# Kernel optimization log

Measured on AMD Instinct MI355X. Metric: run time of the kernel, lower is better.

The kernel has to match this reference:

```python
import jax, jax.numpy as jnp
import numpy as np

B, L, D = 4, 2048, 1024
H = 4096          # hidden_units = 4*D
E = 8             # n_expert
K = 2             # n_expert_activated


def setup_inputs() -> dict:
    key = jax.random.key(0)
    k_x, k_g, k_w1, k_w2 = jax.random.split(key, 4)
    xs = jax.random.normal(k_x, (B, L, D), dtype=jnp.float32)
    gate_w = jax.random.normal(k_g, (E, D), dtype=jnp.float32) * 0.02   # Linear(D->E), no bias
    w1 = jax.random.normal(k_w1, (E, D, H), dtype=jnp.float32) * 0.02   # per-expert w_1 (bias=False)
    w2 = jax.random.normal(k_w2, (E, H, D), dtype=jnp.float32) * 0.02   # per-expert w_2 (bias=False)
    return {"xs": xs, "gate_w": gate_w, "w1": w1, "w2": w2}


def reference(xs, gate_w, w1, w2):
    b, l, d = xs.shape
    x = xs.reshape(-1, d)                                  # (N, D)
    n = x.shape[0]
    router = jnp.einsum('nd,ed->ne', x, gate_w)            # (N, E)
    logits, sel = jax.lax.top_k(router, K)                 # (N, K) each
    weights = jax.nn.softmax(logits.astype(jnp.float32), axis=-1).astype(x.dtype)
    # dense (N, E) combine weights: zero for unselected experts
    dense_w = jnp.zeros((n, E), dtype=x.dtype).at[jnp.arange(n)[:, None], sel].set(weights)
    # dense dispatch: run every expert on every token, zero-weight unselected.
    # Same math as the per-expert gather/scatter loop (dropout inactive at eval).
    h = jax.nn.relu(jnp.einsum('nd,edh->neh', x, w1))      # (N, E, H)
    out = jnp.einsum('neh,ehd,ne->nd', h, w2, dense_w)     # (N, D)
    return out.reshape(b, l, d)
```

## Files before the change

kernel.cpp:

```cpp
#include <hip/hip_runtime.h>
#include <hip/hip_bf16.h>

#define NTOK   8192
#define DDIM   1024
#define HDIM   4096
#define NEXP   8
#define CAP    8192
#define NSLOT  (NTOK * 2)

#define BM 128
#define BN 128
#define BK 64
#define KPAD 72

typedef __attribute__((ext_vector_type(8))) short bf16x8;
typedef __attribute__((ext_vector_type(4))) float f32x4;

__global__ __launch_bounds__(64) void router_kernel(
    const float* __restrict__ xs, const float* __restrict__ gw,
    int* __restrict__ counts, int* __restrict__ toklist, float* __restrict__ wglist)
{
    const int n = blockIdx.x;
    const int lane = threadIdx.x;
    const float* xrow = xs + (size_t)n * DDIM;
    float xv[16];
#pragma unroll
    for (int j = 0; j < 16; ++j) xv[j] = xrow[lane + 64 * j];
    float logit[NEXP];
#pragma unroll
    for (int e = 0; e < NEXP; ++e) {
        float p = 0.f;
        const float* gr = gw + e * DDIM;
#pragma unroll
        for (int j = 0; j < 16; ++j) p += xv[j] * gr[lane + 64 * j];
#pragma unroll
        for (int off = 32; off >= 1; off >>= 1) p += __shfl_xor(p, off);
        logit[e] = p;
    }
    if (lane == 0) {
        int i0 = 0;
#pragma unroll
        for (int e = 1; e < NEXP; ++e) if (logit[e] > logit[i0]) i0 = e;
        int i1 = (i0 == 0) ? 1 : 0;
#pragma unroll
        for (int e = 0; e < NEXP; ++e) if (e != i0 && logit[e] > logit[i1]) i1 = e;
        float ex = expf(logit[i1] - logit[i0]);
        float w0 = 1.f / (1.f + ex);
        float w1 = ex * w0;
        int p0 = atomicAdd(&counts[i0], 1);
        toklist[i0 * CAP + p0] = n;
        wglist[i0 * CAP + p0] = w0;
        int p1 = atomicAdd(&counts[i1], 1);
        toklist[i1 * CAP + p1] = n;
        wglist[i1 * CAP + p1] = w1;
    }
}

__global__ void prefix_kernel(const int* __restrict__ counts, int* __restrict__ base)
{
    if (threadIdx.x == 0 && blockIdx.x == 0) {
        int s = 0;
        for (int e = 0; e < NEXP; ++e) { base[e] = s; s += counts[e]; }
    }
}

__global__ __launch_bounds__(256) void cvt_xs_kernel(
    const float* __restrict__ xs, __hip_bfloat16* __restrict__ xsb)
{
    const size_t i = ((size_t)blockIdx.x * 256 + threadIdx.x) * 8;
    const float4 a = *(const float4*)(xs + i);
    const float4 b = *(const float4*)(xs + i + 4);
    __hip_bfloat16 o[8];
    o[0] = __float2bfloat16(a.x); o[1] = __float2bfloat16(a.y);
    o[2] = __float2bfloat16(a.z); o[3] = __float2bfloat16(a.w);
    o[4] = __float2bfloat16(b.x); o[5] = __float2bfloat16(b.y);
    o[6] = __float2bfloat16(b.z); o[7] = __float2bfloat16(b.w);
    *(bf16x8*)(xsb + i) = *(bf16x8*)o;
}

__global__ __launch_bounds__(256) void transpose_bf16_kernel(
    const float* __restrict__ src, __hip_bfloat16* __restrict__ dst, int R, int C)
{
    __shared__ __hip_bfloat16 t[64][65];
    const int e = blockIdx.z;
    src += (size_t)e * R * C;
    dst += (size_t)e * R * C;
    const int r0 = blockIdx.y * 64, c0 = blockIdx.x * 64;
    const int tid = threadIdx.x;
#pragma unroll
    for (int i = 0; i < 16; ++i) {
        int lin = tid + 256 * i;
        int r = lin >> 6, c = lin & 63;
        t[r][c] = __float2bfloat16(src[(size_t)(r0 + r) * C + c0 + c]);
    }
    __syncthreads();
#pragma unroll
    for (int i = 0; i < 16; ++i) {
        int lin = tid + 256 * i;
        int c = lin >> 6, r = lin & 63;
        dst[(size_t)(c0 + c) * R + r0 + r] = t[r][c];
    }
}

__global__ __launch_bounds__(256) void gemm1_kernel(
    const __hip_bfloat16* __restrict__ xsb, const __hip_bfloat16* __restrict__ w1t,
    const int* __restrict__ counts, const int* __restrict__ base,
    const int* __restrict__ toklist, __hip_bfloat16* __restrict__ h)
{
    const int e = blockIdx.z;
    const int cnt = counts[e];
    const int m0 = blockIdx.y * BM;
    if (m0 >= cnt) return;
    const int n0 = blockIdx.x * BN;

    __shared__ __align__(16) __hip_bfloat16 As[BM * KPAD];
    __shared__ __align__(16) __hip_bfloat16 Bs[BN * KPAD];
    __shared__ int tok_s[BM];

    const int tid = threadIdx.x;
    if (tid < BM) {
        int m = m0 + tid;
        tok_s[tid] = (m < cnt) ? toklist[e * CAP + m] : -1;
    }
    __syncthreads();

    f32x4 acc[4][4];
#pragma unroll
    for (int i = 0; i < 4; ++i)
#pragma unroll
        for (int j = 0; j < 4; ++j) acc[i][j] = (f32x4){0.f, 0.f, 0.f, 0.f};

    const int wave = tid >> 6;
    const int lane = tid & 63;
    const int wm = (wave >> 1) * 64;
    const int wn = (wave & 1) * 64;
    const int l15 = lane & 15;
    const int quad = lane >> 4;
    const int srow = tid >> 3;
    const int soct = (tid & 7) * 8;
    const __hip_bfloat16* w1e = w1t + (size_t)e * HDIM * DDIM;

    for (int k0 = 0; k0 < DDIM; k0 += BK) {
#pragma unroll
        for (int rr = 0; rr < 4; ++rr) {
            int m = srow + rr * 32;
            int t = tok_s[m];
            bf16x8 v = {0, 0, 0, 0, 0, 0, 0, 0};
            if (t >= 0) v = *(const bf16x8*)(xsb + (size_t)t * DDIM + k0 + soct);
            *(bf16x8*)(As + m * KPAD + soct) = v;
        }
#pragma unroll
        for (int rr = 0; rr < 4; ++rr) {
            int n = srow + rr * 32;
            bf16x8 v = *(const bf16x8*)(w1e + (size_t)(n0 + n) * DDIM + k0 + soct);
            *(bf16x8*)(Bs + n * KPAD + soct) = v;
        }
        __syncthreads();
#pragma unroll
        for (int kk = 0; kk < 2; ++kk) {
            bf16x8 a[4], b[4];
#pragma unroll
            for (int i = 0; i < 4; ++i)
                a[i] = *(const bf16x8*)(As + (wm + i * 16 + l15) * KPAD + kk * 32 + quad * 8);
#pragma unroll
            for (int j = 0; j < 4; ++j)
                b[j] = *(const bf16x8*)(Bs + (wn + j * 16 + l15) * KPAD + kk * 32 + quad * 8);
#pragma unroll
            for (int i = 0; i < 4; ++i)
#pragma unroll
                for (int j = 0; j < 4; ++j)
                    acc[i][j] = __builtin_amdgcn_mfma_f32_16x16x32_bf16(a[i], b[j], acc[i][j], 0, 0, 0);
        }
        __syncthreads();
    }

    const int slot0 = base[e] + m0;
#pragma unroll
    for (int i = 0; i < 4; ++i) {
#pragma unroll
        for (int r = 0; r < 4; ++r) {
            int row = wm + i * 16 + quad * 4 + r;
            if (m0 + row < cnt) {
                size_t hrow = (size_t)(slot0 + row) * HDIM + n0 + wn;
#pragma unroll
                for (int j = 0; j < 4; ++j)
                    h[hrow + j * 16 + l15] = __float2bfloat16(fmaxf(acc[i][j][r], 0.f));
            }
        }
    }
}

__global__ __launch_bounds__(256) void gemm2_kernel(
    const __hip_bfloat16* __restrict__ h, const __hip_bfloat16* __restrict__ w2t,
    const int* __restrict__ counts, const int* __restrict__ base,
    const int* __restrict__ toklist, const float* __restrict__ wglist,
    float* __restrict__ out)
{
    const int e = blockIdx.z;
    const int cnt = counts[e];
    const int m0 = blockIdx.y * BM;
    if (m0 >= cnt) return;
    const int n0 = blockIdx.x * BN;

    __shared__ __align__(16) __hip_bfloat16 As[BM * KPAD];
    __shared__ __align__(16) __hip_bfloat16 Bs[BN * KPAD];
    __shared__ int   tok_s[BM];
    __shared__ float wg_s[BM];

    const int tid = threadIdx.x;
    if (tid < BM) {
        int m = m0 + tid;
        tok_s[tid] = (m < cnt) ? toklist[e * CAP + m] : -1;
        wg_s[tid]  = (m < cnt) ? wglist[e * CAP + m] : 0.f;
    }
    __syncthreads();

    f32x4 acc[4][4];
#pragma unroll
    for (int i = 0; i < 4; ++i)
#pragma unroll
        for (int j = 0; j < 4; ++j) acc[i][j] = (f32x4){0.f, 0.f, 0.f, 0.f};

    const int wave = tid >> 6;
    const int lane = tid & 63;
    const int wm = (wave >> 1) * 64;
    const int wn = (wave & 1) * 64;
    const int l15 = lane & 15;
    const int quad = lane >> 4;
    const int srow = tid >> 3;
    const int soct = (tid & 7) * 8;
    const int slot0 = base[e] + m0;
    const __hip_bfloat16* w2e = w2t + (size_t)e * DDIM * HDIM;

    for (int k0 = 0; k0 < HDIM; k0 += BK) {
#pragma unroll
        for (int rr = 0; rr < 4; ++rr) {
            int m = srow + rr * 32;
            bf16x8 v = {0, 0, 0, 0, 0, 0, 0, 0};
            if (m0 + m < cnt) v = *(const bf16x8*)(h + (size_t)(slot0 + m) * HDIM + k0 + soct);
            *(bf16x8*)(As + m * KPAD + soct) = v;
        }
#pragma unroll
        for (int rr = 0; rr < 4; ++rr) {
            int n = srow + rr * 32;
            bf16x8 v = *(const bf16x8*)(w2e + (size_t)(n0 + n) * HDIM + k0 + soct);
            *(bf16x8*)(Bs + n * KPAD + soct) = v;
        }
        __syncthreads();
#pragma unroll
        for (int kk = 0; kk < 2; ++kk) {
            bf16x8 a[4], b[4];
#pragma unroll
            for (int i = 0; i < 4; ++i)
                a[i] = *(const bf16x8*)(As + (wm + i * 16 + l15) * KPAD + kk * 32 + quad * 8);
#pragma unroll
            for (int j = 0; j < 4; ++j)
                b[j] = *(const bf16x8*)(Bs + (wn + j * 16 + l15) * KPAD + kk * 32 + quad * 8);
#pragma unroll
            for (int i = 0; i < 4; ++i)
#pragma unroll
                for (int j = 0; j < 4; ++j)
                    acc[i][j] = __builtin_amdgcn_mfma_f32_16x16x32_bf16(a[i], b[j], acc[i][j], 0, 0, 0);
        }
        __syncthreads();
    }

#pragma unroll
    for (int i = 0; i < 4; ++i) {
#pragma unroll
        for (int r = 0; r < 4; ++r) {
            int row = wm + i * 16 + quad * 4 + r;
            if (m0 + row < cnt) {
                int tok = tok_s[row];
                float w = wg_s[row];
                float* orow = out + (size_t)tok * DDIM + n0 + wn;
#pragma unroll
                for (int j = 0; j < 4; ++j)
                    atomicAdd(&orow[j * 16 + l15], w * acc[i][j][r]);
            }
        }
    }
}

extern "C" void kernel_launch(void* const* d_in, const int* in_sizes, int n_in,
                              void* d_out, int out_size, void* d_ws, size_t ws_size,
                              hipStream_t stream)
{
    const float* xs = (const float*)d_in[0];
    const float* gw = (const float*)d_in[1];
    const float* w1 = (const float*)d_in[2];
    const float* w2 = (const float*)d_in[3];
    float* out = (float*)d_out;

    char* ws = (char*)d_ws;
    size_t o = 0;
    int*   counts  = (int*)(ws + o);  o += 256;
    int*   base    = (int*)(ws + o);  o += 256;
    int*   toklist = (int*)(ws + o);  o += (size_t)NEXP * CAP * 4;
    float* wglist  = (float*)(ws + o); o += (size_t)NEXP * CAP * 4;
    __hip_bfloat16* xsb = (__hip_bfloat16*)(ws + o); o += (size_t)NTOK * DDIM * 2;
    __hip_bfloat16* w1t = (__hip_bfloat16*)(ws + o); o += (size_t)NEXP * DDIM * HDIM * 2;
    __hip_bfloat16* w2t = (__hip_bfloat16*)(ws + o); o += (size_t)NEXP * DDIM * HDIM * 2;
    __hip_bfloat16* hbuf = (__hip_bfloat16*)(ws + o); o += (size_t)NSLOT * HDIM * 2;

    hipMemsetAsync(counts, 0, 256, stream);
    hipMemsetAsync(d_out, 0, (size_t)out_size * sizeof(float), stream);

    router_kernel<<<NTOK, 64, 0, stream>>>(xs, gw, counts, toklist, wglist);
    prefix_kernel<<<1, 64, 0, stream>>>(counts, base);
    cvt_xs_kernel<<<(NTOK * DDIM) / (256 * 8), 256, 0, stream>>>(xs, xsb);
    transpose_bf16_kernel<<<dim3(HDIM / 64, DDIM / 64, NEXP), 256, 0, stream>>>(w1, w1t, DDIM, HDIM);
    transpose_bf16_kernel<<<dim3(DDIM / 64, HDIM / 64, NEXP), 256, 0, stream>>>(w2, w2t, HDIM, DDIM);

    gemm1_kernel<<<dim3(HDIM / BN, CAP / BM, NEXP), 256, 0, stream>>>(
        xsb, w1t, counts, base, toklist, hbuf);
    gemm2_kernel<<<dim3(DDIM / BN, CAP / BM, NEXP), 256, 0, stream>>>(
        hbuf, w2t, counts, base, toklist, wglist, out);
}
```

Baseline: 1.118 ms.

## Use direct global-to-LDS loads in expert GEMMs and vectorize weight transpose

Replaces the register-staged global loads and LDS stores in both expert GEMM kernels with global_load_lds 16-byte direct-to-LDS transfers. This removes the padded LDS layout and precomputes per-lane source pointers, clamping out-of-range rows to the last valid row instead of zero-filling. The weight transpose kernel now reads float4 and writes 4-element bf16 vectors to cut memory transactions. The unpadded LDS layout may add bank conflicts on the MFMA operand reads, and clamped rows load redundant data that the epilogue masks.

```diff
diff --git a/kernel.cpp b/kernel.cpp
--- a/kernel.cpp
+++ b/kernel.cpp
@@ -11,10 +11,13 @@
 #define BM 128
 #define BN 128
 #define BK 64
-#define KPAD 72
 
 typedef __attribute__((ext_vector_type(8))) short bf16x8;
 typedef __attribute__((ext_vector_type(4))) float f32x4;
+
+#define GLD16(g, l) __builtin_amdgcn_global_load_lds(                          \
+    (const __attribute__((address_space(1))) void*)(g),                        \
+    (__attribute__((address_space(3))) void*)(l), 16, 0, 0)
 
 __global__ __launch_bounds__(64) void router_kernel(
     const float* __restrict__ xs, const float* __restrict__ gw,
@@ -81,24 +84,29 @@
 __global__ __launch_bounds__(256) void transpose_bf16_kernel(
     const float* __restrict__ src, __hip_bfloat16* __restrict__ dst, int R, int C)
 {
-    __shared__ __hip_bfloat16 t[64][65];
+    __shared__ __hip_bfloat16 t[64][72];
     const int e = blockIdx.z;
     src += (size_t)e * R * C;
     dst += (size_t)e * R * C;
     const int r0 = blockIdx.y * 64, c0 = blockIdx.x * 64;
     const int tid = threadIdx.x;
 #pragma unroll
-    for (int i = 0; i < 16; ++i) {
-        int lin = tid + 256 * i;
-        int r = lin >> 6, c = lin & 63;
-        t[r][c] = __float2bfloat16(src[(size_t)(r0 + r) * C + c0 + c]);
+    for (int i = 0; i < 4; ++i) {
+        int r = (tid >> 4) + 16 * i;
+        int c = (tid & 15) * 4;
+        float4 v = *(const float4*)(src + (size_t)(r0 + r) * C + c0 + c);
+        t[r][c + 0] = __float2bfloat16(v.x);
+        t[r][c + 1] = __float2bfloat16(v.y);
+        t[r][c + 2] = __float2bfloat16(v.z);
+        t[r][c + 3] = __float2bfloat16(v.w);
     }
     __syncthreads();
 #pragma unroll
-    for (int i = 0; i < 16; ++i) {
-        int lin = tid + 256 * i;
-        int c = lin >> 6, r = lin & 63;
-        dst[(size_t)(c0 + c) * R + r0 + r] = t[r][c];
+    for (int i = 0; i < 4; ++i) {
+        int c = (tid >> 4) + 16 * i;
+        int r = (tid & 15) * 4;
+        __hip_bfloat16 o[4] = { t[r][c], t[r + 1][c], t[r + 2][c], t[r + 3][c] };
+        *(short4*)(dst + (size_t)(c0 + c) * R + r0 + r) = *(short4*)o;
     }
 }
 
@@ -113,47 +121,45 @@
     if (m0 >= cnt) return;
     const int n0 = blockIdx.x * BN;
 
-    __shared__ __align__(16) __hip_bfloat16 As[BM * KPAD];
-    __shared__ __align__(16) __hip_bfloat16 Bs[BN * KPAD];
+    __shared__ __align__(16) __hip_bfloat16 As[BM * BK];
+    __shared__ __align__(16) __hip_bfloat16 Bs[BN * BK];
     __shared__ int tok_s[BM];
 
     const int tid = threadIdx.x;
-    if (tid < BM) {
-        int m = m0 + tid;
-        tok_s[tid] = (m < cnt) ? toklist[e * CAP + m] : -1;
-    }
+    if (tid < BM) tok_s[tid] = toklist[e * CAP + min(m0 + tid, cnt - 1)];
     __syncthreads();
-
-    f32x4 acc[4][4];
-#pragma unroll
-    for (int i = 0; i < 4; ++i)
-#pragma unroll
-        for (int j = 0; j < 4; ++j) acc[i][j] = (f32x4){0.f, 0.f, 0.f, 0.f};
 
     const int wave = tid >> 6;
     const int lane = tid & 63;
+    const int lrow = lane >> 3;
+    const int lcol = (lane & 7) * 8;
+    const __hip_bfloat16* w1e = w1t + (size_t)e * HDIM * DDIM;
+
+    const __hip_bfloat16* srcA[4];
+    const __hip_bfloat16* srcB[4];
+#pragma unroll
+    for (int c = 0; c < 4; ++c) {
+        int r = wave * 32 + c * 8 + lrow;
+        srcA[c] = xsb + (size_t)tok_s[r] * DDIM + lcol;
+        srcB[c] = w1e + (size_t)(n0 + r) * DDIM + lcol;
+    }
+
+    f32x4 acc[4][4];
+#pragma unroll
+    for (int i = 0; i < 4; ++i)
+#pragma unroll
+        for (int j = 0; j < 4; ++j) acc[i][j] = (f32x4){0.f, 0.f, 0.f, 0.f};
+
     const int wm = (wave >> 1) * 64;
     const int wn = (wave & 1) * 64;
     const int l15 = lane & 15;
     const int quad = lane >> 4;
-    const int srow = tid >> 3;
-    const int soct = (tid & 7) * 8;
-    const __hip_bfloat16* w1e = w1t + (size_t)e * HDIM * DDIM;
 
     for (int k0 = 0; k0 < DDIM; k0 += BK) {
 #pragma unroll
-        for (int rr = 0; rr < 4; ++rr) {
-            int m = srow + rr * 32;
-            int t = tok_s[m];
-            bf16x8 v = {0, 0, 0, 0, 0, 0, 0, 0};
-            if (t >= 0) v = *(const bf16x8*)(xsb + (size_t)t * DDIM + k0 + soct);
-            *(bf16x8*)(As + m * KPAD + soct) = v;
-        }
-#pragma unroll
-        for (int rr = 0; rr < 4; ++rr) {
-            int n = srow + rr * 32;
-            bf16x8 v = *(const bf16x8*)(w1e + (size_t)(n0 + n) * DDIM + k0 + soct);
-            *(bf16x8*)(Bs + n * KPAD + soct) = v;
+        for (int c = 0; c < 4; ++c) {
+            GLD16(srcA[c] + k0, As + (wave * 32 + c * 8) * BK);
+            GLD16(srcB[c] + k0, Bs + (wave * 32 + c * 8) * BK);
         }
         __syncthreads();
 #pragma unroll
@@ -161,10 +167,10 @@
             bf16x8 a[4], b[4];
 #pragma unroll
             for (int i = 0; i < 4; ++i)
-                a[i] = *(const bf16x8*)(As + (wm + i * 16 + l15) * KPAD + kk * 32 + quad * 8);
+                a[i] = *(const bf16x8*)(As + (wm + i * 16 + l15) * BK + kk * 32 + quad * 8);
 #pragma unroll
             for (int j = 0; j < 4; ++j)
-                b[j] = *(const bf16x8*)(Bs + (wn + j * 16 + l15) * KPAD + kk * 32 + quad * 8);
+                b[j] = *(const bf16x8*)(Bs + (wn + j * 16 + l15) * BK + kk * 32 + quad * 8);
 #pragma unroll
             for (int i = 0; i < 4; ++i)
 #pragma unroll
@@ -202,8 +208,8 @@
     if (m0 >= cnt) return;
     const int n0 = blockIdx.x * BN;
 
-    __shared__ __align__(16) __hip_bfloat16 As[BM * KPAD];
-    __shared__ __align__(16) __hip_bfloat16 Bs[BN * KPAD];
+    __shared__ __align__(16) __hip_bfloat16 As[BM * BK];
+    __shared__ __align__(16) __hip_bfloat16 Bs[BN * BK];
     __shared__ int   tok_s[BM];
     __shared__ float wg_s[BM];
 
@@ -215,36 +221,38 @@
     }
     __syncthreads();
 
-    f32x4 acc[4][4];
-#pragma unroll
-    for (int i = 0; i < 4; ++i)
-#pragma unroll
-        for (int j = 0; j < 4; ++j) acc[i][j] = (f32x4){0.f, 0.f, 0.f, 0.f};
-
     const int wave = tid >> 6;
     const int lane = tid & 63;
+    const int lrow = lane >> 3;
+    const int lcol = (lane & 7) * 8;
+    const int slot0 = base[e];
+    const __hip_bfloat16* w2e = w2t + (size_t)e * DDIM * HDIM;
+
+    const __hip_bfloat16* srcA[4];
+    const __hip_bfloat16* srcB[4];
+#pragma unroll
+    for (int c = 0; c < 4; ++c) {
+        int r = wave * 32 + c * 8 + lrow;
+        srcA[c] = h + (size_t)(slot0 + min(m0 + r, cnt - 1)) * HDIM + lcol;
+        srcB[c] = w2e + (size_t)(n0 + r) * HDIM + lcol;
+    }
+
+    f32x4 acc[4][4];
+#pragma unroll
+    for (int i = 0; i < 4; ++i)
+#pragma unroll
+        for (int j = 0; j < 4; ++j) acc[i][j] = (f32x4){0.f, 0.f, 0.f, 0.f};
+
     const int wm = (wave >> 1) * 64;
     const int wn = (wave & 1) * 64;
     const int l15 = lane & 15;
     const int quad = lane >> 4;
-    const int srow = tid >> 3;
-    const int soct = (tid & 7) * 8;
-    const int slot0 = base[e] + m0;
-    const __hip_bfloat16* w2e = w2t + (size_t)e * DDIM * HDIM;
 
     for (int k0 = 0; k0 < HDIM; k0 += BK) {
 #pragma unroll
-        for (int rr = 0; rr < 4; ++rr) {
-            int m = srow + rr * 32;
-            bf16x8 v = {0, 0, 0, 0, 0, 0, 0, 0};
-            if (m0 + m < cnt) v = *(const bf16x8*)(h + (size_t)(slot0 + m) * HDIM + k0 + soct);
-            *(bf16x8*)(As + m * KPAD + soct) = v;
-        }
-#pragma unroll
-        for (int rr = 0; rr < 4; ++rr) {
-            int n = srow + rr * 32;
-            bf16x8 v = *(const bf16x8*)(w2e + (size_t)(n0 + n) * HDIM + k0 + soct);
-            *(bf16x8*)(Bs + n * KPAD + soct) = v;
+        for (int c = 0; c < 4; ++c) {
+            GLD16(srcA[c] + k0, As + (wave * 32 + c * 8) * BK);
+            GLD16(srcB[c] + k0, Bs + (wave * 32 + c * 8) * BK);
         }
         __syncthreads();
 #pragma unroll
@@ -252,10 +260,10 @@
             bf16x8 a[4], b[4];
 #pragma unroll
             for (int i = 0; i < 4; ++i)
-                a[i] = *(const bf16x8*)(As + (wm + i * 16 + l15) * KPAD + kk * 32 + quad * 8);
+                a[i] = *(const bf16x8*)(As + (wm + i * 16 + l15) * BK + kk * 32 + quad * 8);
 #pragma unroll
             for (int j = 0; j < 4; ++j)
-                b[j] = *(const bf16x8*)(Bs + (wn + j * 16 + l15) * KPAD + kk * 32 + quad * 8);
+                b[j] = *(const bf16x8*)(Bs + (wn + j * 16 + l15) * BK + kk * 32 + quad * 8);
 #pragma unroll
             for (int i = 0; i < 4; ++i)
 #pragma unroll
```

After: 1.098 ms. No clear change (-1.7%).
